# Kernel tuning notes

Hardware: AMD Instinct MI355X
Metric: run time of the kernel (lower is better)

## Reference

```python
import jax, jax.numpy as jnp
import numpy as np

N = 20000          # nodes
E = 320000         # edges
C = 64             # channel multiplicity (64x0e node feats)
NATTR = 10         # node attr (species one-hot) dim
EDGE_FEAT = 8      # radial bessel features
L_DIMS = (1, 3, 5) # irrep dims for l = 0,1,2
RAD = [64, 64, 64]
AVG_NEIGH = 16.0
NUM_L = len(L_DIMS)


def setup_inputs() -> dict:
    key = jax.random.key(0)
    ks = jax.random.split(key, 12)
    node_attrs = jax.random.uniform(ks[0], (N, NATTR), dtype=jnp.float32)
    node_feats = jax.random.normal(ks[1], (N, C), dtype=jnp.float32)
    edge_attrs = jax.random.normal(ks[2], (E, sum(L_DIMS)), dtype=jnp.float32)
    edge_feats = jax.random.normal(ks[3], (E, EDGE_FEAT), dtype=jnp.float32)
    edge_index = jax.random.randint(ks[4], (2, E), 0, N, dtype=jnp.int64)
    # linear1: o3.Linear(64x0e -> 64x0e)
    W_lin1 = jax.random.normal(ks[5], (C, C), dtype=jnp.float32)
    # radial MLP: FullyConnectedNet([8,64,64,64,192], Identity)
    W_r0 = jax.random.normal(ks[6], (EDGE_FEAT, RAD[0]), dtype=jnp.float32)
    W_r1 = jax.random.normal(ks[7], (RAD[0], RAD[1]), dtype=jnp.float32)
    W_r2 = jax.random.normal(ks[8], (RAD[1], RAD[2]), dtype=jnp.float32)
    W_r3 = jax.random.normal(ks[9], (RAD[2], NUM_L * C), dtype=jnp.float32)
    # post-aggregation linear: o3.Linear(64x0e+64x1o+64x2e -> same), per-l 64x64 mix
    W_msg = jax.random.normal(ks[10], (NUM_L, C, C), dtype=jnp.float32)
    # skip_tp: FullyConnectedTensorProduct(64x0e, 10x0e -> 64x0e), 'uvw'
    W_skip = jax.random.normal(ks[11], (C, NATTR, C), dtype=jnp.float32)
    return {
        "node_attrs": node_attrs, "node_feats": node_feats,
        "edge_attrs": edge_attrs, "edge_feats": edge_feats,
        "edge_index": edge_index,
        "W_lin1": W_lin1, "W_r0": W_r0, "W_r1": W_r1, "W_r2": W_r2,
        "W_r3": W_r3, "W_msg": W_msg, "W_skip": W_skip,
    }


def reference(node_attrs, node_feats, edge_attrs, edge_feats, edge_index,
              W_lin1, W_r0, W_r1, W_r2, W_r3, W_msg, W_skip):
    sender, receiver = edge_index[0], edge_index[1]
    num_nodes = node_feats.shape[0]
    num_edges = edge_feats.shape[0]

    # linear1 (o3.Linear on scalars): fan_in normalized
    h = node_feats @ (W_lin1 / np.float32(np.sqrt(C)))           # [N, C]

    # radial MLP (e3nn FullyConnectedNet, identity activation)
    w = edge_feats
    for W in (W_r0, W_r1, W_r2, W_r3):
        w = w @ (W / np.float32(np.sqrt(W.shape[0])))
    tp_w = w.reshape(num_edges, NUM_L, C)                        # per-l 'uvu' weights

    # edge gather + weighted tensor product (0e x l -> l per channel)
    xs = h[sender]                                               # [E, C]
    blocks = []
    off = 0
    for l, d in enumerate(L_DIMS):
        y_l = edge_attrs[:, off:off + d]                         # [E, d]
        m_l = (xs * tp_w[:, l, :])[:, :, None] * y_l[:, None, :] # [E, C, d]
        blocks.append(m_l.reshape(num_edges, C * d))
        off += d
    mji = jnp.concatenate(blocks, axis=-1)                       # [E, C*9]

    # scatter-sum to receivers
    msg = jax.ops.segment_sum(mji, receiver, num_segments=num_nodes)  # [N, C*9]

    # per-l linear mix + avg-neighbor norm, then reshape_irreps -> [N, C, 9]
    out_blocks = []
    off = 0
    for l, d in enumerate(L_DIMS):
        m_l = msg[:, off:off + C * d].reshape(num_nodes, C, d)
        o_l = jnp.einsum('num,uv->nvm', m_l, W_msg[l]) / np.float32(np.sqrt(C))
        out_blocks.append(o_l)
        off += C * d
    out = jnp.concatenate(out_blocks, axis=-1) / np.float32(AVG_NEIGH)  # [N, C, 9]

    # self connection: FullyConnectedTensorProduct(64x0e, 10x0e -> 64x0e)
    sc = jnp.einsum('nu,nv,uvw->nw', h, node_attrs, W_skip) / np.float32(np.sqrt(C * NATTR))
    return out, sc
```

## Files before the change

### kernel.cpp

```cpp
#include <hip/hip_runtime.h>

#define N_NODES 20000
#define N_EDGES 320000
#define C 64
#define NATTR 10
#define MSG_DIM 576
#define WC_COLS 192
#define PRE 12

__global__ void node_linear_hist(const float* __restrict__ nf,
                                 const float* __restrict__ W,
                                 float* __restrict__ h,
                                 const int* __restrict__ eidx,
                                 int* __restrict__ counts) {
    const int t = threadIdx.x;
    {
        const int e = blockIdx.x * 256 + t;
        atomicAdd(&counts[eidx[N_EDGES + e]], 1);
    }
    __shared__ float Ws[64 * 64];
    __shared__ float row[4][64];
    const int lane = t & 63, wv = t >> 6;
    for (int i = t; i < 4096; i += 256) Ws[i] = W[i] * 0.125f;
    __syncthreads();
    const int base = blockIdx.x * 16;
    for (int it = 0; it < 4; ++it) {
        int n = base + it * 4 + wv;
        if (n >= N_NODES) break;
        row[wv][lane] = nf[(size_t)n * 64 + lane];
        float acc = 0.f;
        #pragma unroll
        for (int k = 0; k < 64; ++k) acc += row[wv][k] * Ws[k * 64 + lane];
        h[(size_t)n * 64 + lane] = acc;
    }
}

#define SCAN_PER 20
__global__ __launch_bounds__(1024) void scan_radial_kernel(
        const int* __restrict__ counts,
        int* __restrict__ start, int* __restrict__ cursor,
        const float* __restrict__ Wr0, const float* __restrict__ Wr1,
        const float* __restrict__ Wr2, const float* __restrict__ Wr3,
        float* __restrict__ Wc, float* __restrict__ rec, int ST) {
    __shared__ int wsum[16];
    __shared__ float T[8 * 64];
    __shared__ float T2[8 * 64];
    const int t = threadIdx.x, lane = t & 63, w = t >> 6;
    const float s0r = 0.35355339059327373f;
    const float s1r = 0.125f;

    const int base = t * SCAN_PER;
    int v[SCAN_PER];
    int s = 0;
    #pragma unroll
    for (int j = 0; j < SCAN_PER; ++j) {
        const int idx = base + j;
        v[j] = (idx < N_NODES) ? counts[idx] : 0;
        s += v[j];
    }
    int sc = s;
    #pragma unroll
    for (int off = 1; off < 64; off <<= 1) {
        int up = __shfl_up(sc, off);
        if (lane >= off) sc += up;
    }
    if (lane == 63) wsum[w] = sc;
    if (t < 16) rec[(size_t)(N_EDGES + t) * ST + 17] = 0.f;
    for (int i = t; i < 8 * 64; i += 1024) {
        int r = i >> 6, c2 = i & 63;
        float acc = 0.f;
        for (int k = 0; k < 64; ++k) acc += Wr0[r * 64 + k] * Wr1[k * 64 + c2];
        T[i] = acc * (s0r * s1r);
    }
    __syncthreads();
    if (t == 0) {
        int a = 0;
        #pragma unroll
        for (int i = 0; i < 16; ++i) { int x = wsum[i]; wsum[i] = a; a += x; }
    }
    for (int i = t; i < 8 * 64; i += 1024) {
        int r = i >> 6, c2 = i & 63;
        float acc = 0.f;
        for (int k = 0; k < 64; ++k) acc += T[r * 64 + k] * Wr2[k * 64 + c2];
        T2[i] = acc * s1r;
    }
    __syncthreads();
    int a = wsum[w] + (sc - s);
    #pragma unroll
    for (int j = 0; j < SCAN_PER; ++j) {
        const int idx = base + j;
        if (idx < N_NODES) {
            start[idx] = a;
            cursor[idx] = a;
            a += v[j];
        }
    }
    for (int i = t; i < 8 * WC_COLS; i += 1024) {
        int r = i / WC_COLS, c2 = i % WC_COLS;
        float acc = 0.f;
        for (int k = 0; k < 64; ++k) acc += T2[r * 64 + k] * Wr3[k * WC_COLS + c2];
        Wc[i] = acc * s1r;
    }
}

template<int ST>
__global__ void scatter_build(const int* __restrict__ eidx,
                              const float* __restrict__ ef,
                              const float* __restrict__ ea,
                              int* __restrict__ cursor,
                              float* __restrict__ rec) {
    const int e = blockIdx.x * 256 + threadIdx.x;
    if (e >= N_EDGES) return;
    const int r = eidx[N_EDGES + e];
    const int s = eidx[e];
    const int pos = atomicAdd(&cursor[r], 1);
    const float4* f4 = reinterpret_cast<const float4*>(ef + (size_t)e * 8);
    const float* y = ea + (size_t)e * 9;
    float4* o = reinterpret_cast<float4*>(rec + (size_t)pos * ST);
    o[0] = f4[0];
    o[1] = f4[1];
    o[2] = make_float4(y[0], y[1], y[2], y[3]);
    o[3] = make_float4(y[4], y[5], y[6], y[7]);
    o[4] = make_float4(y[8], __int_as_float(s), 0.f, 0.f);
    if (ST == 32) {
        const float4 z = make_float4(0.f, 0.f, 0.f, 0.f);
        o[5] = z; o[6] = z; o[7] = z;
    }
}

template<int ST>
__global__ __launch_bounds__(256) void gather_sorted(
                              const float* __restrict__ rec,
                              const float* __restrict__ h,
                              const float* __restrict__ Wc,
                              const int* __restrict__ start,
                              const int* __restrict__ counts,
                              float* __restrict__ msg) {
    __shared__ float part[2][9][64];
    const int t = threadIdx.x, lane = t & 63, wv = t >> 6;
    const int g = wv >> 1;
    const int half = wv & 1;
    const int n = blockIdx.x * 2 + g;

    float wc0[8], wc1[8], wc2[8];
    #pragma unroll
    for (int k = 0; k < 8; ++k) {
        wc0[k] = Wc[k * WC_COLS + lane];
        wc1[k] = Wc[k * WC_COLS + 64 + lane];
        wc2[k] = Wc[k * WC_COLS + 128 + lane];
    }

    float p0 = 0.f;
    float p1[3] = {0.f, 0.f, 0.f};
    float p2[5] = {0.f, 0.f, 0.f, 0.f, 0.f};

    if (n < N_NODES) {
        const int s0 = start[n], cnt = counts[n];
        const int jbeg = half ? (cnt >> 1) : 0;
        const int jend = half ? cnt : (cnt >> 1);
        const int m = jend - jbeg;
        const int base = s0 + jbeg;

        if (m > 0) {
            const int P = (m < PRE) ? m : PRE;
            int snd[PRE];
            #pragma unroll
            for (int b = 0; b < PRE; ++b)
                snd[b] = __float_as_int(rec[(size_t)(base + b) * ST + 17]);
            float xs[PRE];
            #pragma unroll
            for (int b = 0; b < PRE; ++b) {
                const int sb = (b < P) ? snd[b] : snd[0];
                xs[b] = h[(size_t)sb * 64 + lane];
            }
            #pragma unroll
            for (int jj = 0; jj < PRE / 2; ++jj) {
                const int j = jj * 2;
                if (j < P) {
                    const bool has2 = (j + 1 < P);
                    const int j1 = has2 ? (j + 1) : j;
                    const float gate1 = has2 ? 1.f : 0.f;
                    const float4* q0 = reinterpret_cast<const float4*>(rec + (size_t)(base + j) * ST);
                    const float4* q1 = reinterpret_cast<const float4*>(rec + (size_t)(base + j1) * ST);
                    const float4 e00 = q0[0], e01 = q0[1];
                    const float4 a00 = q0[2], a01 = q0[3], a02 = q0[4];
                    const float4 e10 = q1[0], e11 = q1[1];
                    const float4 a10 = q1[2], a11 = q1[3], a12 = q1[4];
                    const float xa = xs[j];
                    const float xb = (has2 ? xs[j + 1] : 0.f) * gate1;
                    {
                        const float* fk = reinterpret_cast<const float*>(&e00);
                        const float* gk = reinterpret_cast<const float*>(&e01);
                        float w0 = fk[0] * wc0[0], w1 = fk[0] * wc1[0], w2 = fk[0] * wc2[0];
                        #pragma unroll
                        for (int k = 1; k < 4; ++k) {
                            w0 += fk[k] * wc0[k]; w1 += fk[k] * wc1[k]; w2 += fk[k] * wc2[k];
                        }
                        #pragma unroll
                        for (int k = 0; k < 4; ++k) {
                            w0 += gk[k] * wc0[k + 4]; w1 += gk[k] * wc1[k + 4]; w2 += gk[k] * wc2[k + 4];
                        }
                        const float b0 = xa * w0, b1 = xa * w1, b2 = xa * w2;
                        p0    += b0 * a00.x;
                        p1[0] += b1 * a00.y; p1[1] += b1 * a00.z; p1[2] += b1 * a00.w;
                        p2[0] += b2 * a01.x; p2[1] += b2 * a01.y; p2[2] += b2 * a01.z;
                        p2[3] += b2 * a01.w; p2[4] += b2 * a02.x;
                    }
                    {
                        const float* fk = reinterpret_cast<const float*>(&e10);
                        const float* gk = reinterpret_cast<const float*>(&e11);
                        float w0 = fk[0] * wc0[0], w1 = fk[0] * wc1[0], w2 = fk[0] * wc2[0];
                        #pragma unroll
                        for (int k = 1; k < 4; ++k) {
                            w0 += fk[k] * wc0[k]; w1 += fk[k] * wc1[k]; w2 += fk[k] * wc2[k];
                        }
                        #pragma unroll
                        for (int k = 0; k < 4; ++k) {
                            w0 += gk[k] * wc0[k + 4]; w1 += gk[k] * wc1[k + 4]; w2 += gk[k] * wc2[k + 4];
                        }
                        const float b0 = xb * w0, b1 = xb * w1, b2 = xb * w2;
                        p0    += b0 * a10.x;
                        p1[0] += b1 * a10.y; p1[1] += b1 * a10.z; p1[2] += b1 * a10.w;
                        p2[0] += b2 * a11.x; p2[1] += b2 * a11.y; p2[2] += b2 * a11.z;
                        p2[3] += b2 * a11.w; p2[4] += b2 * a12.x;
                    }
                }
            }
            for (int j = PRE; j < m; ++j) {
                const float4* q = reinterpret_cast<const float4*>(rec + (size_t)(base + j) * ST);
                const float4 fa = q[0], fb = q[1];
                const float4 ya = q[2], yb = q[3], yc = q[4];
                const int snd_t = __float_as_int(yc.y);
                const float xs_t = h[(size_t)snd_t * 64 + lane];
                const float* fk = reinterpret_cast<const float*>(&fa);
                const float* gk = reinterpret_cast<const float*>(&fb);
                float w0 = fk[0] * wc0[0], w1 = fk[0] * wc1[0], w2 = fk[0] * wc2[0];
                #pragma unroll
                for (int k = 1; k < 4; ++k) {
                    w0 += fk[k] * wc0[k]; w1 += fk[k] * wc1[k]; w2 += fk[k] * wc2[k];
                }
                #pragma unroll
                for (int k = 0; k < 4; ++k) {
                    w0 += gk[k] * wc0[k + 4]; w1 += gk[k] * wc1[k + 4]; w2 += gk[k] * wc2[k + 4];
                }
                const float b0 = xs_t * w0, b1 = xs_t * w1, b2 = xs_t * w2;
                p0    += b0 * ya.x;
                p1[0] += b1 * ya.y; p1[1] += b1 * ya.z; p1[2] += b1 * ya.w;
                p2[0] += b2 * yb.x; p2[1] += b2 * yb.y; p2[2] += b2 * yb.z;
                p2[3] += b2 * yb.w; p2[4] += b2 * yc.x;
            }
        }
    }

    if (half) {
        part[g][0][lane] = p0;
        #pragma unroll
        for (int m2 = 0; m2 < 3; ++m2) part[g][1 + m2][lane] = p1[m2];
        #pragma unroll
        for (int m2 = 0; m2 < 5; ++m2) part[g][4 + m2][lane] = p2[m2];
    }
    __syncthreads();
    if (!half && n < N_NODES) {
        float* mrow = msg + (size_t)n * MSG_DIM;
        mrow[lane] = p0 + part[g][0][lane];
        #pragma unroll
        for (int m2 = 0; m2 < 3; ++m2)
            mrow[64 + lane * 3 + m2] = p1[m2] + part[g][1 + m2][lane];
        #pragma unroll
        for (int m2 = 0; m2 < 5; ++m2)
            mrow[256 + lane * 5 + m2] = p2[m2] + part[g][4 + m2][lane];
    }
}

__global__ __launch_bounds__(256) void out_transform(
        const float* __restrict__ Wmsg,
        float* __restrict__ out) {
    __shared__ __align__(16) float stage[8 * MSG_DIM];
    const int t = threadIdx.x, lane = t & 63, wv = t >> 6;
    {
        const float4* src = reinterpret_cast<const float4*>(
            out + (size_t)blockIdx.x * 8 * MSG_DIM);
        float4* dst = reinterpret_cast<float4*>(stage);
        #pragma unroll
        for (int i = 0; i < 4; ++i) dst[t + 256 * i] = src[t + 256 * i];
        if (t < 128) dst[t + 1024] = src[t + 1024];
    }
    __syncthreads();
    const float scale = 1.f / 128.f;

    const int r0 = wv * 2;
    const float* rowA = stage + (size_t)r0 * MSG_DIM;
    const float* rowB = rowA + MSG_DIM;
    float oA[9] = {0.f, 0.f, 0.f, 0.f, 0.f, 0.f, 0.f, 0.f, 0.f};
    float oB[9] = {0.f, 0.f, 0.f, 0.f, 0.f, 0.f, 0.f, 0.f, 0.f};

    #pragma unroll 1
    for (int c = 0; c < 16; ++c) {
        const int u0 = c * 4;
        float w0[4], w1[4], w2[4];
        #pragma unroll
        for (int k = 0; k < 4; ++k) {
            w0[k] = Wmsg[(u0 + k) * 64 + lane];
            w1[k] = Wmsg[4096 + (u0 + k) * 64 + lane];
            w2[k] = Wmsg[8192 + (u0 + k) * 64 + lane];
        }
        #pragma unroll
        for (int rr = 0; rr < 2; ++rr) {
            const float* row = rr ? rowB : rowA;
            float* o = rr ? oB : oA;
            const float4 c0 = *reinterpret_cast<const float4*>(row + u0);
            const float4 c1a = *reinterpret_cast<const float4*>(row + 64 + u0 * 3);
            const float4 c1b = *reinterpret_cast<const float4*>(row + 64 + u0 * 3 + 4);
            const float4 c1c = *reinterpret_cast<const float4*>(row + 64 + u0 * 3 + 8);
            const float4 c2a = *reinterpret_cast<const float4*>(row + 256 + u0 * 5);
            const float4 c2b = *reinterpret_cast<const float4*>(row + 256 + u0 * 5 + 4);
            const float4 c2c = *reinterpret_cast<const float4*>(row + 256 + u0 * 5 + 8);
            const float4 c2d = *reinterpret_cast<const float4*>(row + 256 + u0 * 5 + 12);
            const float4 c2e = *reinterpret_cast<const float4*>(row + 256 + u0 * 5 + 16);
            o[0] += c0.x * w0[0] + c0.y * w0[1] + c0.z * w0[2] + c0.w * w0[3];
            o[1] += c1a.x * w1[0] + c1a.w * w1[1] + c1b.z * w1[2] + c1c.y * w1[3];
            o[2] += c1a.y * w1[0] + c1b.x * w1[1] + c1b.w * w1[2] + c1c.z * w1[3];
            o[3] += c1a.z * w1[0] + c1b.y * w1[1] + c1c.x * w1[2] + c1c.w * w1[3];
            o[4] += c2a.x * w2[0] + c2b.y * w2[1] + c2c.z * w2[2] + c2d.w * w2[3];
            o[5] += c2a.y * w2[0] + c2b.z * w2[1] + c2c.w * w2[2] + c2e.x * w2[3];
            o[6] += c2a.z * w2[0] + c2b.w * w2[1] + c2d.x * w2[2] + c2e.y * w2[3];
            o[7] += c2a.w * w2[0] + c2c.x * w2[1] + c2d.y * w2[2] + c2e.z * w2[3];
            o[8] += c2b.x * w2[0] + c2c.y * w2[1] + c2d.z * w2[2] + c2e.w * w2[3];
        }
    }
    float* opA = out + ((size_t)blockIdx.x * 8 + r0) * MSG_DIM + lane * 9;
    float* opB = opA + MSG_DIM;
    #pragma unroll
    for (int m = 0; m < 9; ++m) opA[m] = oA[m] * scale;
    #pragma unroll
    for (int m = 0; m < 9; ++m) opB[m] = oB[m] * scale;
}

__global__ __launch_bounds__(256) void skip_kernel(
                            const float* __restrict__ h,
                            const float* __restrict__ attrs,
                            const float* __restrict__ Wskip,
                            float* __restrict__ sc) {
    __shared__ float hl[32 * 64];
    const int t = threadIdx.x, lane = t & 63, wv = t >> 6;
    const int nb = blockIdx.x * 32;
    for (int i = t; i < 32 * 64; i += 256) hl[i] = h[(size_t)(nb + (i >> 6)) * 64 + (i & 63)];
    __syncthreads();

    float alr[8][NATTR];
    #pragma unroll
    for (int i = 0; i < 8; ++i) {
        const float* ap = attrs + (size_t)(nb + wv + 4 * i) * NATTR;
        #pragma unroll
        for (int v = 0; v < NATTR; ++v) alr[i][v] = ap[v];
    }

    float acc[8] = {0.f, 0.f, 0.f, 0.f, 0.f, 0.f, 0.f, 0.f};
    #pragma unroll 1
    for (int u4 = 0; u4 < 16; ++u4) {
        const int u0 = u4 * 4;
        float4 hu[8];
        #pragma unroll
        for (int i = 0; i < 8; ++i)
            hu[i] = *reinterpret_cast<const float4*>(&hl[(wv + 4 * i) * 64 + u0]);
        #pragma unroll
        for (int uu = 0; uu < 4; ++uu) {
            float tmp[8] = {0.f, 0.f, 0.f, 0.f, 0.f, 0.f, 0.f, 0.f};
            #pragma unroll
            for (int v = 0; v < NATTR; ++v) {
                const float wk = Wskip[((u0 + uu) * NATTR + v) * 64 + lane];
                #pragma unroll
                for (int i = 0; i < 8; ++i) tmp[i] += alr[i][v] * wk;
            }
            #pragma unroll
            for (int i = 0; i < 8; ++i) {
                const float huv = (uu == 0) ? hu[i].x : (uu == 1) ? hu[i].y
                                 : (uu == 2) ? hu[i].z : hu[i].w;
                acc[i] += huv * tmp[i];
            }
        }
    }
    const float scale = 0.03952847075210474f;
    #pragma unroll
    for (int i = 0; i < 8; ++i)
        sc[(size_t)(nb + wv + 4 * i) * 64 + lane] = acc[i] * scale;
}

extern "C" void kernel_launch(void* const* d_in, const int* in_sizes, int n_in,
                              void* d_out, int out_size, void* d_ws, size_t ws_size,
                              hipStream_t stream) {
    const float* node_attrs = (const float*)d_in[0];
    const float* node_feats = (const float*)d_in[1];
    const float* edge_attrs = (const float*)d_in[2];
    const float* edge_feats = (const float*)d_in[3];
    const int*   edge_index = (const int*)d_in[4];
    const float* W_lin1 = (const float*)d_in[5];
    const float* W_r0 = (const float*)d_in[6];
    const float* W_r1 = (const float*)d_in[7];
    const float* W_r2 = (const float*)d_in[8];
    const float* W_r3 = (const float*)d_in[9];
    const float* W_msg = (const float*)d_in[10];
    const float* W_skip = (const float*)d_in[11];

    float* out = (float*)d_out;
    float* sc  = out + (size_t)N_NODES * MSG_DIM;

    float* wsf = (float*)d_ws;
    float* Wc = wsf;
    float* h  = wsf + 2048;
    int* wsi   = (int*)(wsf + 2048 + (size_t)N_NODES * 64);
    int* counts = wsi;
    int* start  = wsi + N_NODES;
    int* cursor = wsi + 2 * N_NODES;
    float* rec  = (float*)(wsi + 3 * N_NODES);

    const size_t head_bytes = ((size_t)2048 + (size_t)N_NODES * 64) * 4
                            + (size_t)(3 * N_NODES) * 4;
    const size_t need32 = head_bytes + (size_t)(N_EDGES + 16) * 32 * 4;
    const bool wide = (ws_size >= need32);

    hipMemsetAsync(counts, 0, N_NODES * sizeof(int), stream);
    node_linear_hist<<<1250, 256, 0, stream>>>(node_feats, W_lin1, h,
                                               edge_index, counts);
    scan_radial_kernel<<<1, 1024, 0, stream>>>(counts, start, cursor,
                                               W_r0, W_r1, W_r2, W_r3, Wc,
                                               rec, wide ? 32 : 20);
    if (wide) {
        scatter_build<32><<<1250, 256, 0, stream>>>(
            edge_index, edge_feats, edge_attrs, cursor, rec);
        gather_sorted<32><<<(N_NODES + 1) / 2, 256, 0, stream>>>(
            rec, h, Wc, start, counts, out);
    } else {
        scatter_build<20><<<1250, 256, 0, stream>>>(
            edge_index, edge_feats, edge_attrs, cursor, rec);
        gather_sorted<20><<<(N_NODES + 1) / 2, 256, 0, stream>>>(
            rec, h, Wc, start, counts, out);
    }

    out_transform<<<2500, 256, 0, stream>>>(W_msg, out);
    skip_kernel<<<625, 256, 0, stream>>>(h, node_attrs, W_skip, sc);
}
```

Before: 248.6 us.

## Fuse skip tensor product into node linear kernel and fix record stride

Moves the skip-connection tensor product into the node-linear/histogram kernel, so h is reused straight from shared memory and one launch plus a global reload of h go away. The edge record stride is fixed at 20 floats instead of the 32-float padded layout that was chosen when the workspace was large enough, which cuts scatter and gather traffic at the cost of 16-byte-unaligned records. out_transform now handles 16 rows per block instead of 8, with four rows per wave. The fused kernel now does more work per block, which may lower its occupancy.

```diff
diff --git a/kernel.cpp b/kernel.cpp
--- a/kernel.cpp
+++ b/kernel.cpp
@@ -7,12 +7,17 @@
 #define MSG_DIM 576
 #define WC_COLS 192
 #define PRE 12
-
-__global__ void node_linear_hist(const float* __restrict__ nf,
-                                 const float* __restrict__ W,
-                                 float* __restrict__ h,
-                                 const int* __restrict__ eidx,
-                                 int* __restrict__ counts) {
+#define REC 20
+
+__global__ __launch_bounds__(256) void node_linear_hist_skip(
+        const float* __restrict__ nf,
+        const float* __restrict__ W,
+        float* __restrict__ h,
+        const int* __restrict__ eidx,
+        int* __restrict__ counts,
+        const float* __restrict__ attrs,
+        const float* __restrict__ Wskip,
+        float* __restrict__ sc) {
     const int t = threadIdx.x;
     {
         const int e = blockIdx.x * 256 + t;
@@ -20,19 +25,60 @@
     }
     __shared__ float Ws[64 * 64];
     __shared__ float row[4][64];
+    __shared__ float hl[16][64];
     const int lane = t & 63, wv = t >> 6;
     for (int i = t; i < 4096; i += 256) Ws[i] = W[i] * 0.125f;
     __syncthreads();
     const int base = blockIdx.x * 16;
+    #pragma unroll 1
     for (int it = 0; it < 4; ++it) {
-        int n = base + it * 4 + wv;
-        if (n >= N_NODES) break;
+        const int nl = it * 4 + wv;
+        const int n = base + nl;
         row[wv][lane] = nf[(size_t)n * 64 + lane];
         float acc = 0.f;
         #pragma unroll
         for (int k = 0; k < 64; ++k) acc += row[wv][k] * Ws[k * 64 + lane];
         h[(size_t)n * 64 + lane] = acc;
-    }
+        hl[nl][lane] = acc;
+    }
+    __syncthreads();
+
+    float alr[4][NATTR];
+    #pragma unroll
+    for (int i = 0; i < 4; ++i) {
+        const float* ap = attrs + (size_t)(base + wv + 4 * i) * NATTR;
+        #pragma unroll
+        for (int v = 0; v < NATTR; ++v) alr[i][v] = ap[v];
+    }
+    float acc[4] = {0.f, 0.f, 0.f, 0.f};
+    #pragma unroll 1
+    for (int u4 = 0; u4 < 16; ++u4) {
+        const int u0 = u4 * 4;
+        float4 hu[4];
+        #pragma unroll
+        for (int i = 0; i < 4; ++i)
+            hu[i] = *reinterpret_cast<const float4*>(&hl[wv + 4 * i][u0]);
+        #pragma unroll
+        for (int uu = 0; uu < 4; ++uu) {
+            float tmp[4] = {0.f, 0.f, 0.f, 0.f};
+            #pragma unroll
+            for (int v = 0; v < NATTR; ++v) {
+                const float wk = Wskip[((u0 + uu) * NATTR + v) * 64 + lane];
+                #pragma unroll
+                for (int i = 0; i < 4; ++i) tmp[i] += alr[i][v] * wk;
+            }
+            #pragma unroll
+            for (int i = 0; i < 4; ++i) {
+                const float huv = (uu == 0) ? hu[i].x : (uu == 1) ? hu[i].y
+                                 : (uu == 2) ? hu[i].z : hu[i].w;
+                acc[i] += huv * tmp[i];
+            }
+        }
+    }
+    const float scale = 0.03952847075210474f;
+    #pragma unroll
+    for (int i = 0; i < 4; ++i)
+        sc[(size_t)(base + wv + 4 * i) * 64 + lane] = acc[i] * scale;
 }
 
 #define SCAN_PER 20
@@ -41,7 +87,7 @@
         int* __restrict__ start, int* __restrict__ cursor,
         const float* __restrict__ Wr0, const float* __restrict__ Wr1,
         const float* __restrict__ Wr2, const float* __restrict__ Wr3,
-        float* __restrict__ Wc, float* __restrict__ rec, int ST) {
+        float* __restrict__ Wc, float* __restrict__ rec) {
     __shared__ int wsum[16];
     __shared__ float T[8 * 64];
     __shared__ float T2[8 * 64];
@@ -65,7 +111,7 @@
         if (lane >= off) sc += up;
     }
     if (lane == 63) wsum[w] = sc;
-    if (t < 16) rec[(size_t)(N_EDGES + t) * ST + 17] = 0.f;
+    if (t < 16) rec[(size_t)(N_EDGES + t) * REC + 17] = 0.f;
     for (int i = t; i < 8 * 64; i += 1024) {
         int r = i >> 6, c2 = i & 63;
         float acc = 0.f;
@@ -103,7 +149,6 @@
     }
 }
 
-template<int ST>
 __global__ void scatter_build(const int* __restrict__ eidx,
                               const float* __restrict__ ef,
                               const float* __restrict__ ea,
@@ -116,19 +161,14 @@
     const int pos = atomicAdd(&cursor[r], 1);
     const float4* f4 = reinterpret_cast<const float4*>(ef + (size_t)e * 8);
     const float* y = ea + (size_t)e * 9;
-    float4* o = reinterpret_cast<float4*>(rec + (size_t)pos * ST);
+    float4* o = reinterpret_cast<float4*>(rec + (size_t)pos * REC);
     o[0] = f4[0];
     o[1] = f4[1];
     o[2] = make_float4(y[0], y[1], y[2], y[3]);
     o[3] = make_float4(y[4], y[5], y[6], y[7]);
     o[4] = make_float4(y[8], __int_as_float(s), 0.f, 0.f);
-    if (ST == 32) {
-        const float4 z = make_float4(0.f, 0.f, 0.f, 0.f);
-        o[5] = z; o[6] = z; o[7] = z;
-    }
-}
-
-template<int ST>
+}
+
 __global__ __launch_bounds__(256) void gather_sorted(
                               const float* __restrict__ rec,
                               const float* __restrict__ h,
@@ -166,7 +206,7 @@
             int snd[PRE];
             #pragma unroll
             for (int b = 0; b < PRE; ++b)
-                snd[b] = __float_as_int(rec[(size_t)(base + b) * ST + 17]);
+                snd[b] = __float_as_int(rec[(size_t)(base + b) * REC + 17]);
             float xs[PRE];
             #pragma unroll
             for (int b = 0; b < PRE; ++b) {
@@ -180,8 +220,8 @@
                     const bool has2 = (j + 1 < P);
                     const int j1 = has2 ? (j + 1) : j;
                     const float gate1 = has2 ? 1.f : 0.f;
-                    const float4* q0 = reinterpret_cast<const float4*>(rec + (size_t)(base + j) * ST);
-                    const float4* q1 = reinterpret_cast<const float4*>(rec + (size_t)(base + j1) * ST);
+                    const float4* q0 = reinterpret_cast<const float4*>(rec + (size_t)(base + j) * REC);
+                    const float4* q1 = reinterpret_cast<const float4*>(rec + (size_t)(base + j1) * REC);
                     const float4 e00 = q0[0], e01 = q0[1];
                     const float4 a00 = q0[2], a01 = q0[3], a02 = q0[4];
                     const float4 e10 = q1[0], e11 = q1[1];
@@ -227,7 +267,7 @@
                 }
             }
             for (int j = PRE; j < m; ++j) {
-                const float4* q = reinterpret_cast<const float4*>(rec + (size_t)(base + j) * ST);
+                const float4* q = reinterpret_cast<const float4*>(rec + (size_t)(base + j) * REC);
                 const float4 fa = q[0], fb = q[1];
                 const float4 ya = q[2], yb = q[3], yc = q[4];
                 const int snd_t = __float_as_int(yc.y);
@@ -275,25 +315,20 @@
 __global__ __launch_bounds__(256) void out_transform(
         const float* __restrict__ Wmsg,
         float* __restrict__ out) {
-    __shared__ __align__(16) float stage[8 * MSG_DIM];
+    __shared__ __align__(16) float stage[16 * MSG_DIM];
     const int t = threadIdx.x, lane = t & 63, wv = t >> 6;
     {
         const float4* src = reinterpret_cast<const float4*>(
-            out + (size_t)blockIdx.x * 8 * MSG_DIM);
+            out + (size_t)blockIdx.x * 16 * MSG_DIM);
         float4* dst = reinterpret_cast<float4*>(stage);
         #pragma unroll
-        for (int i = 0; i < 4; ++i) dst[t + 256 * i] = src[t + 256 * i];
-        if (t < 128) dst[t + 1024] = src[t + 1024];
+        for (int i = 0; i < 9; ++i) dst[t + 256 * i] = src[t + 256 * i];
     }
     __syncthreads();
     const float scale = 1.f / 128.f;
 
-    const int r0 = wv * 2;
-    const float* rowA = stage + (size_t)r0 * MSG_DIM;
-    const float* rowB = rowA + MSG_DIM;
-    float oA[9] = {0.f, 0.f, 0.f, 0.f, 0.f, 0.f, 0.f, 0.f, 0.f};
-    float oB[9] = {0.f, 0.f, 0.f, 0.f, 0.f, 0.f, 0.f, 0.f, 0.f};
-
+    const int r0 = wv * 4;
+    float o[4][9] = {};
     #pragma unroll 1
     for (int c = 0; c < 16; ++c) {
         const int u0 = c * 4;
@@ -305,9 +340,9 @@
             w2[k] = Wmsg[8192 + (u0 + k) * 64 + lane];
         }
         #pragma unroll
-        for (int rr = 0; rr < 2; ++rr) {
-            const float* row = rr ? rowB : rowA;
-            float* o = rr ? oB : oA;
+        for (int rr = 0; rr < 4; ++rr) {
+            const float* row = stage + (size_t)(r0 + rr) * MSG_DIM;
+            float* o9 = o[rr];
             const float4 c0 = *reinterpret_cast<const float4*>(row + u0);
             const float4 c1a = *reinterpret_cast<const float4*>(row + 64 + u0 * 3);
             const float4 c1b = *reinterpret_cast<const float4*>(row + 64 + u0 * 3 + 4);
@@ -317,73 +352,23 @@
             const float4 c2c = *reinterpret_cast<const float4*>(row + 256 + u0 * 5 + 8);
             const float4 c2d = *reinterpret_cast<const float4*>(row + 256 + u0 * 5 + 12);
             const float4 c2e = *reinterpret_cast<const float4*>(row + 256 + u0 * 5 + 16);
-            o[0] += c0.x * w0[0] + c0.y * w0[1] + c0.z * w0[2] + c0.w * w0[3];
-            o[1] += c1a.x * w1[0] + c1a.w * w1[1] + c1b.z * w1[2] + c1c.y * w1[3];
-            o[2] += c1a.y * w1[0] + c1b.x * w1[1] + c1b.w * w1[2] + c1c.z * w1[3];
-            o[3] += c1a.z * w1[0] + c1b.y * w1[1] + c1c.x * w1[2] + c1c.w * w1[3];
-            o[4] += c2a.x * w2[0] + c2b.y * w2[1] + c2c.z * w2[2] + c2d.w * w2[3];
-            o[5] += c2a.y * w2[0] + c2b.z * w2[1] + c2c.w * w2[2] + c2e.x * w2[3];
-            o[6] += c2a.z * w2[0] + c2b.w * w2[1] + c2d.x * w2[2] + c2e.y * w2[3];
-            o[7] += c2a.w * w2[0] + c2c.x * w2[1] + c2d.y * w2[2] + c2e.z * w2[3];
-            o[8] += c2b.x * w2[0] + c2c.y * w2[1] + c2d.z * w2[2] + c2e.w * w2[3];
+            o9[0] += c0.x * w0[0] + c0.y * w0[1] + c0.z * w0[2] + c0.w * w0[3];
+            o9[1] += c1a.x * w1[0] + c1a.w * w1[1] + c1b.z * w1[2] + c1c.y * w1[3];
+            o9[2] += c1a.y * w1[0] + c1b.x * w1[1] + c1b.w * w1[2] + c1c.z * w1[3];
+            o9[3] += c1a.z * w1[0] + c1b.y * w1[1] + c1c.x * w1[2] + c1c.w * w1[3];
+            o9[4] += c2a.x * w2[0] + c2b.y * w2[1] + c2c.z * w2[2] + c2d.w * w2[3];
+            o9[5] += c2a.y * w2[0] + c2b.z * w2[1] + c2c.w * w2[2] + c2e.x * w2[3];
+            o9[6] += c2a.z * w2[0] + c2b.w * w2[1] + c2d.x * w2[2] + c2e.y * w2[3];
+            o9[7] += c2a.w * w2[0] + c2c.x * w2[1] + c2d.y * w2[2] + c2e.z * w2[3];
+            o9[8] += c2b.x * w2[0] + c2c.y * w2[1] + c2d.z * w2[2] + c2e.w * w2[3];
         }
     }
-    float* opA = out + ((size_t)blockIdx.x * 8 + r0) * MSG_DIM + lane * 9;
-    float* opB = opA + MSG_DIM;
-    #pragma unroll
-    for (int m = 0; m < 9; ++m) opA[m] = oA[m] * scale;
-    #pragma unroll
-    for (int m = 0; m < 9; ++m) opB[m] = oB[m] * scale;
-}
-
-__global__ __launch_bounds__(256) void skip_kernel(
-                            const float* __restrict__ h,
-                            const float* __restrict__ attrs,
-                            const float* __restrict__ Wskip,
-                            float* __restrict__ sc) {
-    __shared__ float hl[32 * 64];
-    const int t = threadIdx.x, lane = t & 63, wv = t >> 6;
-    const int nb = blockIdx.x * 32;
-    for (int i = t; i < 32 * 64; i += 256) hl[i] = h[(size_t)(nb + (i >> 6)) * 64 + (i & 63)];
-    __syncthreads();
-
-    float alr[8][NATTR];
-    #pragma unroll
-    for (int i = 0; i < 8; ++i) {
-        const float* ap = attrs + (size_t)(nb + wv + 4 * i) * NATTR;
-        #pragma unroll
-        for (int v = 0; v < NATTR; ++v) alr[i][v] = ap[v];
-    }
-
-    float acc[8] = {0.f, 0.f, 0.f, 0.f, 0.f, 0.f, 0.f, 0.f};
-    #pragma unroll 1
-    for (int u4 = 0; u4 < 16; ++u4) {
-        const int u0 = u4 * 4;
-        float4 hu[8];
-        #pragma unroll
-        for (int i = 0; i < 8; ++i)
-            hu[i] = *reinterpret_cast<const float4*>(&hl[(wv + 4 * i) * 64 + u0]);
-        #pragma unroll
-        for (int uu = 0; uu < 4; ++uu) {
-            float tmp[8] = {0.f, 0.f, 0.f, 0.f, 0.f, 0.f, 0.f, 0.f};
-            #pragma unroll
-            for (int v = 0; v < NATTR; ++v) {
-                const float wk = Wskip[((u0 + uu) * NATTR + v) * 64 + lane];
-                #pragma unroll
-                for (int i = 0; i < 8; ++i) tmp[i] += alr[i][v] * wk;
-            }
-            #pragma unroll
-            for (int i = 0; i < 8; ++i) {
-                const float huv = (uu == 0) ? hu[i].x : (uu == 1) ? hu[i].y
-                                 : (uu == 2) ? hu[i].z : hu[i].w;
-                acc[i] += huv * tmp[i];
-            }
-        }
-    }
-    const float scale = 0.03952847075210474f;
-    #pragma unroll
-    for (int i = 0; i < 8; ++i)
-        sc[(size_t)(nb + wv + 4 * i) * 64 + lane] = acc[i] * scale;
+    #pragma unroll
+    for (int rr = 0; rr < 4; ++rr) {
+        float* op = out + ((size_t)blockIdx.x * 16 + r0 + rr) * MSG_DIM + lane * 9;
+        #pragma unroll
+        for (int m = 0; m < 9; ++m) op[m] = o[rr][m] * scale;
+    }
 }
 
 extern "C" void kernel_launch(void* const* d_in, const int* in_sizes, int n_in,
@@ -414,29 +399,15 @@
     int* cursor = wsi + 2 * N_NODES;
     float* rec  = (float*)(wsi + 3 * N_NODES);
 
-    const size_t head_bytes = ((size_t)2048 + (size_t)N_NODES * 64) * 4
-                            + (size_t)(3 * N_NODES) * 4;
-    const size_t need32 = head_bytes + (size_t)(N_EDGES + 16) * 32 * 4;
-    const bool wide = (ws_size >= need32);
-
     hipMemsetAsync(counts, 0, N_NODES * sizeof(int), stream);
-    node_linear_hist<<<1250, 256, 0, stream>>>(node_feats, W_lin1, h,
-                                               edge_index, counts);
+    node_linear_hist_skip<<<1250, 256, 0, stream>>>(node_feats, W_lin1, h,
+                                                    edge_index, counts,
+                                                    node_attrs, W_skip, sc);
     scan_radial_kernel<<<1, 1024, 0, stream>>>(counts, start, cursor,
-                                               W_r0, W_r1, W_r2, W_r3, Wc,
-                                               rec, wide ? 32 : 20);
-    if (wide) {
-        scatter_build<32><<<1250, 256, 0, stream>>>(
-            edge_index, edge_feats, edge_attrs, cursor, rec);
-        gather_sorted<32><<<(N_NODES + 1) / 2, 256, 0, stream>>>(
-            rec, h, Wc, start, counts, out);
-    } else {
-        scatter_build<20><<<1250, 256, 0, stream>>>(
-            edge_index, edge_feats, edge_attrs, cursor, rec);
-        gather_sorted<20><<<(N_NODES + 1) / 2, 256, 0, stream>>>(
-            rec, h, Wc, start, counts, out);
-    }
-
-    out_transform<<<2500, 256, 0, stream>>>(W_msg, out);
-    skip_kernel<<<625, 256, 0, stream>>>(h, node_attrs, W_skip, sc);
-}
+                                               W_r0, W_r1, W_r2, W_r3, Wc, rec);
+    scatter_build<<<1250, 256, 0, stream>>>(
+        edge_index, edge_feats, edge_attrs, cursor, rec);
+    gather_sorted<<<(N_NODES + 1) / 2, 256, 0, stream>>>(
+        rec, h, Wc, start, counts, out);
+    out_transform<<<1250, 256, 0, stream>>>(W_msg, out);
+}
```

Result: no change. 251.0 us (+1.0%).
